# Kernel tuning notes

Hardware: AMD Instinct MI355X
Metric: run time of the kernel (lower is better)

## Reference

```python
import jax, jax.numpy as jnp
import numpy as np

B = 4096          # batch_size
D_EMB = 16        # per-side embedding dim (embed_to_from width = 2*D_EMB)
D_HIGH = 784      # flattened high-dim feature size
NSR = 5           # negative_sample_rate
A = 1.576943      # UMAP _a
B_PARAM = 0.8950608  # UMAP _b
REPULSION = 1.0
EPS = 1e-4
GLOBAL_LOSS = 0.5
TOTAL_STEPS = 1000
BATCH_COUNT = 500  # fixed step for deterministic alpha/beta
WARMUP = int(0.05 * TOTAL_STEPS)


def _safe_sqrt(sq):
    # sqrt with zero (not NaN) gradient at 0, matching zero-distance pairs
    safe = jnp.where(sq > 0, sq, 1.0)
    return jnp.where(sq > 0, jnp.sqrt(safe), 0.0)


def _pairwise_dist(x):
    # ||x_i - x_j|| via gram trick; avoids materializing [N,N,D]
    sq = jnp.sum(x * x, axis=1)                      # [N]
    gram = x @ x.T                                   # [N,N]
    d2 = sq[:, None] + sq[None, :] - 2.0 * gram
    return _safe_sqrt(jnp.maximum(d2, 0.0))


def _umap_ce_loss(embed_to_from, perm):
    e_to, e_from = jnp.split(embed_to_from, 2, axis=1)   # [B, D_EMB] each
    neg_to = jnp.repeat(e_to, NSR, axis=0)               # [B*NSR, D_EMB]
    repeat_neg = jnp.repeat(e_from, NSR, axis=0)
    neg_from = repeat_neg[perm]                          # shuffled negatives
    d_pos = _safe_sqrt(jnp.sum((e_to - e_from) ** 2, axis=1))
    d_neg = _safe_sqrt(jnp.sum((neg_to - neg_from) ** 2, axis=1))
    dist = jnp.concatenate([d_pos, d_neg], axis=0)       # [B*(1+NSR)]
    p_dist = 1.0 / (1.0 + A * dist ** (2.0 * B_PARAM))
    p_graph = jnp.concatenate([jnp.ones(B, p_dist.dtype), jnp.zeros(B * NSR, p_dist.dtype)])
    attraction = -p_graph * jnp.log(jnp.clip(p_dist, EPS, 1.0))
    repellant = -(1.0 - p_graph) * jnp.log(jnp.clip(1.0 - p_dist, EPS, 1.0)) * REPULSION
    return jnp.mean(attraction + repellant)


def _global_feature_loss(embed_to_from, to_x):
    e_to = embed_to_from[:, :D_EMB]
    to_x = to_x.reshape(to_x.shape[0], -1)
    high_dis = _pairwise_dist(to_x)     # [N,N]
    low_dis = _pairwise_dist(e_to)      # [N,N]
    # row-wise pearson correlation between high_dis and low_dis
    h = high_dis - jnp.mean(high_dis, axis=1, keepdims=True)
    l = low_dis - jnp.mean(low_dis, axis=1, keepdims=True)
    num = jnp.sum(h * l, axis=1)
    den = jnp.sqrt(jnp.sum(h * h, axis=1)) * jnp.sqrt(jnp.sum(l * l, axis=1))
    corr = jnp.mean(num / den)
    return -corr


def _alpha_beta():
    if BATCH_COUNT >= WARMUP:
        if BATCH_COUNT <= 0.9 * TOTAL_STEPS:
            beta = max(0.0, GLOBAL_LOSS * (1 - BATCH_COUNT / (TOTAL_STEPS - WARMUP * 4)) ** 2)
        else:
            beta = 0.0
        alpha = max(0.0, 1 - beta)
    else:
        alpha = 0.0
        beta = GLOBAL_LOSS
    return alpha, beta


def setup_inputs() -> dict:
    key = jax.random.key(0)
    k1, k2, k3 = jax.random.split(key, 3)
    embed_to_from = jax.random.normal(k1, (B, 2 * D_EMB), dtype=jnp.float32)
    placeholder = jax.random.normal(k2, (B, D_HIGH), dtype=jnp.float32)
    perm = jax.random.permutation(k3, B * NSR).astype(jnp.int32)
    return {"embed_to_from": embed_to_from, "placeholder": placeholder, "perm": perm}


def reference(embed_to_from, placeholder, perm):
    loss = _umap_ce_loss(embed_to_from, perm)
    loss_g = _global_feature_loss(embed_to_from, placeholder)
    alpha, beta = _alpha_beta()
    return alpha * loss + beta * loss_g
```

## Files before the change

### kernel.cpp

```cpp
#include <hip/hip_runtime.h>
#include <hip/hip_bf16.h>
#include <math.h>

#define NB    4096
#define DH    784
#define KX    800
#define NSR   5
#define NNEG  (NB*NSR)
#define NTOT  (NB + NNEG)

#define A_CONST 1.576943f
#define PEXP    1.7901216f
#define EPS_C   1.0e-4f
#define ALPHA_C 0.9296875f
#define BETA_C  0.0703125f

#define NSLOT 64
#define SLAB  (NB * NSLOT)
#define NBLK  528
#define BUFE  4096

typedef __hip_bfloat16 bf16;
typedef short bf16x8 __attribute__((ext_vector_type(8)));
typedef float f32x4  __attribute__((ext_vector_type(4)));

#define WS_XBF    0
#define WS_EBF    6553600
#define WS_SQX    6815744
#define WS_SQE    6832128
#define WS_STATSP 6848512
#define WS_UPART  12091392
#define WS_CPART  12091776

__device__ __forceinline__ void gl2lds16(const bf16* g, bf16* l) {
    __builtin_amdgcn_global_load_lds(
        (const __attribute__((address_space(1))) unsigned int*)g,
        (__attribute__((address_space(3))) unsigned int*)l,
        16, 0, 0);
}

__global__ void prep_fused(const float* __restrict__ X, const float* __restrict__ emb,
                           const int* __restrict__ perm, bf16* __restrict__ Xbf,
                           float* __restrict__ sqx, bf16* __restrict__ Ebf,
                           float* __restrict__ sqe, float* __restrict__ upart) {
    if (blockIdx.x < 1024) {
        const int wave = threadIdx.x >> 6, lane = threadIdx.x & 63;
        const int row = blockIdx.x * 4 + wave;
        const float4* xr = (const float4*)(X + (size_t)row * DH);
        bf16* xb = Xbf + (size_t)row * KX;
        float s = 0.f;
        #pragma unroll
        for (int it = 0; it < 4; ++it) {
            const int idx = lane + it * 64;
            if (idx < 196) {
                float4 v = xr[idx];
                s += v.x * v.x + v.y * v.y + v.z * v.z + v.w * v.w;
                union { bf16 h[4]; ushort4 u; } cv;
                cv.h[0] = __float2bfloat16(v.x);
                cv.h[1] = __float2bfloat16(v.y);
                cv.h[2] = __float2bfloat16(v.z);
                cv.h[3] = __float2bfloat16(v.w);
                *(ushort4*)(xb + idx * 4) = cv.u;
            }
        }
        if (lane < 16) xb[DH + lane] = __float2bfloat16(0.f);
        #pragma unroll
        for (int off = 32; off; off >>= 1) s += __shfl_down(s, off, 64);
        if (lane == 0) sqx[row] = s;
        return;
    }
    const int ub = blockIdx.x - 1024;
    const int t = ub * 256 + threadIdx.x;
    float val = 0.f;
    if (t < NB) {
        const float4* av = (const float4*)(emb + (size_t)t * 32);
        float4 t0 = av[0], t1 = av[1], t2 = av[2], t3 = av[3];
        float4 f0 = av[4], f1 = av[5], f2 = av[6], f3 = av[7];
        bf16* eb = Ebf + (size_t)t * 32;
        union { bf16 h[4]; ushort4 u; } cv;
        #define ST4(dst, q) cv.h[0]=__float2bfloat16(q.x); cv.h[1]=__float2bfloat16(q.y); \
                            cv.h[2]=__float2bfloat16(q.z); cv.h[3]=__float2bfloat16(q.w); \
                            *(ushort4*)(dst) = cv.u;
        ST4(eb,      t0) ST4(eb + 4,  t1) ST4(eb + 8,  t2) ST4(eb + 12, t3)
        #undef ST4
        ushort4 z = {0, 0, 0, 0};
        *(ushort4*)(eb + 16) = z; *(ushort4*)(eb + 20) = z;
        *(ushort4*)(eb + 24) = z; *(ushort4*)(eb + 28) = z;
        sqe[t] = t0.x*t0.x + t0.y*t0.y + t0.z*t0.z + t0.w*t0.w
               + t1.x*t1.x + t1.y*t1.y + t1.z*t1.z + t1.w*t1.w
               + t2.x*t2.x + t2.y*t2.y + t2.z*t2.z + t2.w*t2.w
               + t3.x*t3.x + t3.y*t3.y + t3.z*t3.z + t3.w*t3.w;
        float d2 = 0.f;
        #define D2(a, b) { float4 df = {a.x-b.x, a.y-b.y, a.z-b.z, a.w-b.w}; \
                           d2 += df.x*df.x + df.y*df.y + df.z*df.z + df.w*df.w; }
        D2(t0, f0) D2(t1, f1) D2(t2, f2) D2(t3, f3)
        #undef D2
        float d = sqrtf(d2);
        float p = 1.f / (1.f + A_CONST * powf(d, PEXP));
        val = -logf(fminf(fmaxf(p, EPS_C), 1.f));
    } else if (t < NTOT) {
        const int k = t - NB;
        const int ti = k / 5;
        const int fi = perm[k] / 5;
        const float4* at = (const float4*)(emb + (size_t)ti * 32);
        const float4* bt = (const float4*)(emb + (size_t)fi * 32 + 16);
        float d2 = 0.f;
        #pragma unroll
        for (int q = 0; q < 4; ++q) {
            float4 a = at[q], b = bt[q];
            float4 df = {a.x-b.x, a.y-b.y, a.z-b.z, a.w-b.w};
            d2 += df.x*df.x + df.y*df.y + df.z*df.z + df.w*df.w;
        }
        float d = sqrtf(d2);
        float p = 1.f / (1.f + A_CONST * powf(d, PEXP));
        val = -logf(fminf(fmaxf(1.f - p, EPS_C), 1.f));
    }
    #pragma unroll
    for (int off = 32; off; off >>= 1) val += __shfl_down(val, off, 64);
    __shared__ float ps[4];
    if ((threadIdx.x & 63) == 0) ps[threadIdx.x >> 6] = val;
    __syncthreads();
    if (threadIdx.x == 0) upart[ub] = ps[0] + ps[1] + ps[2] + ps[3];
}

__global__ __launch_bounds__(256, 3) void gram_kernel(
    const bf16* __restrict__ Xbf, const bf16* __restrict__ Ebf,
    const float* __restrict__ sqx, const float* __restrict__ sqe,
    float* __restrict__ statsp) {
    __shared__ bf16 As[2 * BUFE];
    __shared__ bf16 Bs[2 * BUFE];
    __shared__ float sqxs[256];
    __shared__ float sqes[256];

    int n = (blockIdx.x & 7) * 66 + (blockIdx.x >> 3);
    int bi = 0;
    while (n >= 32 - bi) { n -= 32 - bi; ++bi; }
    const int bj = bi + n;
    const int i0 = bi * 128, j0 = bj * 128;

    const int tid  = threadIdx.x;
    const int wave = tid >> 6;
    const int lane = tid & 63;
    const int wy = wave >> 1, wx = wave & 1;
    const int quad = lane >> 4, l15 = lane & 15;

    f32x4 acc[4][4];
    #pragma unroll
    for (int a = 0; a < 4; ++a)
        #pragma unroll
        for (int b = 0; b < 4; ++b)
            acc[a][b] = (f32x4){0.f, 0.f, 0.f, 0.f};

    const int c0  = wave * 2;
    const int rA  = lane >> 2;
    const int gseg = ((lane & 3) ^ ((lane >> 3) & 3)) * 8;

    const bf16* gA0 = Xbf + (size_t)(i0 + c0 * 16 + rA) * KX + gseg;
    const bf16* gA1 = Xbf + (size_t)(i0 + c0 * 16 + 16 + rA) * KX + gseg;
    const bf16* gB0 = Xbf + (size_t)(j0 + c0 * 16 + rA) * KX + gseg;
    const bf16* gB1 = Xbf + (size_t)(j0 + c0 * 16 + 16 + rA) * KX + gseg;

    gl2lds16(gA0, As + c0 * 512);
    gl2lds16(gA1, As + c0 * 512 + 512);
    gl2lds16(gB0, Bs + c0 * 512);
    gl2lds16(gB1, Bs + c0 * 512 + 512);
    gA0 += 32; gA1 += 32; gB0 += 32; gB1 += 32;

    if (tid < 128) {
        sqxs[tid] = sqx[i0 + tid]; sqxs[128 + tid] = sqx[j0 + tid];
        sqes[tid] = sqe[i0 + tid]; sqes[128 + tid] = sqe[j0 + tid];
    }

    const int posq = (quad ^ ((l15 >> 1) & 3)) * 8;

    for (int it = 0; it < 25; ++it) {
        __syncthreads();
        const int cur = (it & 1) * BUFE;
        const int nxt = ((it + 1) & 1) * BUFE;
        if (it < 24) {
            gl2lds16(gA0, As + nxt + c0 * 512);
            gl2lds16(gA1, As + nxt + c0 * 512 + 512);
            gl2lds16(gB0, Bs + nxt + c0 * 512);
            gl2lds16(gB1, Bs + nxt + c0 * 512 + 512);
            gA0 += 32; gA1 += 32; gB0 += 32; gB1 += 32;
        } else {
            gl2lds16(Ebf + (size_t)(i0 + c0 * 16 + rA) * 32 + gseg,      As + nxt + c0 * 512);
            gl2lds16(Ebf + (size_t)(i0 + c0 * 16 + 16 + rA) * 32 + gseg, As + nxt + c0 * 512 + 512);
            gl2lds16(Ebf + (size_t)(j0 + c0 * 16 + rA) * 32 + gseg,      Bs + nxt + c0 * 512);
            gl2lds16(Ebf + (size_t)(j0 + c0 * 16 + 16 + rA) * 32 + gseg, Bs + nxt + c0 * 512 + 512);
        }
        bf16x8 af[4], bfr[4];
        #pragma unroll
        for (int mi = 0; mi < 4; ++mi)
            af[mi] = *(const bf16x8*)&As[cur + (wy * 64 + mi * 16 + l15) * 32 + posq];
        #pragma unroll
        for (int ni = 0; ni < 4; ++ni)
            bfr[ni] = *(const bf16x8*)&Bs[cur + (wx * 64 + ni * 16 + l15) * 32 + posq];
        #pragma unroll
        for (int mi = 0; mi < 4; ++mi)
            #pragma unroll
            for (int ni = 0; ni < 4; ++ni)
                acc[mi][ni] = __builtin_amdgcn_mfma_f32_16x16x32_bf16(
                    af[mi], bfr[ni], acc[mi][ni], 0, 0, 0);
    }
    __syncthreads();

    const int slot_r = bj * 2 + wx;
    const int slot_c = bi * 2 + wy;
    bf16x8 bfrE[4];
    #pragma unroll
    for (int ni = 0; ni < 4; ++ni)
        bfrE[ni] = *(const bf16x8*)&Bs[BUFE + (wx * 64 + ni * 16 + l15) * 32 + posq];
    float cH[4] = {0,0,0,0}, cH2[4] = {0,0,0,0}, cL[4] = {0,0,0,0},
          cL2[4] = {0,0,0,0}, cHL[4] = {0,0,0,0};
    #pragma unroll
    for (int mi = 0; mi < 4; ++mi) {
        bf16x8 afE = *(const bf16x8*)&As[BUFE + (wy * 64 + mi * 16 + l15) * 32 + posq];
        f32x4 aE[4];
        #pragma unroll
        for (int ni = 0; ni < 4; ++ni) {
            f32x4 z = (f32x4){0.f, 0.f, 0.f, 0.f};
            aE[ni] = __builtin_amdgcn_mfma_f32_16x16x32_bf16(afE, bfrE[ni], z, 0, 0, 0);
        }
        const int ilocb = wy * 64 + mi * 16 + quad * 4;
        float sH[4] = {0,0,0,0}, sH2[4] = {0,0,0,0}, sL[4] = {0,0,0,0},
              sL2[4] = {0,0,0,0}, sHL[4] = {0,0,0,0};
        #pragma unroll
        for (int ni = 0; ni < 4; ++ni) {
            const int jloc = wx * 64 + ni * 16 + l15;
            const int j = j0 + jloc;
            const float sqxj = sqxs[128 + jloc];
            const float sqej = sqes[128 + jloc];
            #pragma unroll
            for (int r = 0; r < 4; ++r) {
                const int iloc = ilocb + r;
                const int i = i0 + iloc;
                float H, L;
                if (i == j) { H = 0.f; L = 0.f; }
                else {
                    float d2  = sqxs[iloc] + sqxj - 2.0f * acc[mi][ni][r];
                    H = sqrtf(fmaxf(d2, 0.f));
                    float d2e = sqes[iloc] + sqej - 2.0f * aE[ni][r];
                    L = sqrtf(fmaxf(d2e, 0.f));
                }
                sH[r] += H; sH2[r] += H * H; sL[r] += L; sL2[r] += L * L; sHL[r] += H * L;
                cH[ni] += H; cH2[ni] += H * H; cL[ni] += L; cL2[ni] += L * L; cHL[ni] += H * L;
            }
        }
        #pragma unroll
        for (int r = 0; r < 4; ++r) {
            float v0 = sH[r], v1 = sH2[r], v2 = sL[r], v3 = sL2[r], v4 = sHL[r];
            #pragma unroll
            for (int off = 1; off < 16; off <<= 1) {
                v0 += __shfl_xor(v0, off, 64);
                v1 += __shfl_xor(v1, off, 64);
                v2 += __shfl_xor(v2, off, 64);
                v3 += __shfl_xor(v3, off, 64);
                v4 += __shfl_xor(v4, off, 64);
            }
            if (l15 == 0) {
                const int i = i0 + ilocb + r;
                float* base = statsp + (size_t)slot_r * NB + i;
                base[0 * SLAB] = v0;
                base[1 * SLAB] = v1;
                base[2 * SLAB] = v2;
                base[3 * SLAB] = v3;
                base[4 * SLAB] = v4;
            }
        }
    }
    if (bi != bj) {
        #pragma unroll
        for (int ni = 0; ni < 4; ++ni) {
            float v0 = cH[ni], v1 = cH2[ni], v2 = cL[ni], v3 = cL2[ni], v4 = cHL[ni];
            #pragma unroll
            for (int off = 16; off < 64; off <<= 1) {
                v0 += __shfl_xor(v0, off, 64);
                v1 += __shfl_xor(v1, off, 64);
                v2 += __shfl_xor(v2, off, 64);
                v3 += __shfl_xor(v3, off, 64);
                v4 += __shfl_xor(v4, off, 64);
            }
            if (quad == 0) {
                const int j = j0 + wx * 64 + ni * 16 + l15;
                float* base = statsp + (size_t)slot_c * NB + j;
                base[0 * SLAB] = v0;
                base[1 * SLAB] = v1;
                base[2 * SLAB] = v2;
                base[3 * SLAB] = v3;
                base[4 * SLAB] = v4;
            }
        }
    }
}

__global__ void finish1_kernel(const float* __restrict__ statsp, float* __restrict__ cpart) {
    __shared__ float ps2[4][64][5];
    const int t = threadIdx.x;
    const int rloc = t & 63;
    const int sg = t >> 6;
    const int r = blockIdx.x * 64 + rloc;
    float sh = 0.f, sh2 = 0.f, sl = 0.f, sl2 = 0.f, shl = 0.f;
    for (int s = sg * 16; s < sg * 16 + 16; ++s) {
        const float* base = statsp + (size_t)s * NB + r;
        sh  += base[0 * SLAB];
        sh2 += base[1 * SLAB];
        sl  += base[2 * SLAB];
        sl2 += base[3 * SLAB];
        shl += base[4 * SLAB];
    }
    ps2[sg][rloc][0] = sh; ps2[sg][rloc][1] = sh2; ps2[sg][rloc][2] = sl;
    ps2[sg][rloc][3] = sl2; ps2[sg][rloc][4] = shl;
    __syncthreads();
    if (t < 64) {
        float a = 0.f, b = 0.f, c = 0.f, d = 0.f, e = 0.f;
        #pragma unroll
        for (int g = 0; g < 4; ++g) {
            a += ps2[g][t][0]; b += ps2[g][t][1]; c += ps2[g][t][2];
            d += ps2[g][t][3]; e += ps2[g][t][4];
        }
        const float invN = 1.0f / (float)NB;
        float num = e - a * c * invN;
        float vh  = fmaxf(b - a * a * invN, 0.f);
        float vl  = fmaxf(d - c * c * invN, 0.f);
        float local = num / (sqrtf(vh) * sqrtf(vl));
        #pragma unroll
        for (int off = 32; off; off >>= 1) local += __shfl_down(local, off, 64);
        if (t == 0) cpart[blockIdx.x] = local;
    }
}

__global__ void final_kernel(const float* __restrict__ cpart, const float* __restrict__ upart,
                             float* __restrict__ out) {
    const int t = threadIdx.x;
    float c = (t < 64) ? cpart[t] : 0.f;
    float u = (t < 96) ? upart[t] : 0.f;
    #pragma unroll
    for (int off = 32; off; off >>= 1) {
        c += __shfl_down(c, off, 64);
        u += __shfl_down(u, off, 64);
    }
    __shared__ float pc[2], pu[2];
    if ((t & 63) == 0) { pc[t >> 6] = c; pu[t >> 6] = u; }
    __syncthreads();
    if (t == 0) {
        float corr = (pc[0] + pc[1]) / (float)NB;
        float loss_g = -corr;
        float loss_u = (pu[0] + pu[1]) / (float)NTOT;
        out[0] = ALPHA_C * loss_u + BETA_C * loss_g;
    }
}

extern "C" void kernel_launch(void* const* d_in, const int* in_sizes, int n_in,
                              void* d_out, int out_size, void* d_ws, size_t ws_size,
                              hipStream_t stream) {
    const float* emb  = (const float*)d_in[0];
    const float* ph   = (const float*)d_in[1];
    const int*   perm = (const int*)d_in[2];
    float* out = (float*)d_out;

    char* ws = (char*)d_ws;
    bf16*  Xbf    = (bf16*) (ws + WS_XBF);
    bf16*  Ebf    = (bf16*) (ws + WS_EBF);
    float* sqx    = (float*)(ws + WS_SQX);
    float* sqe    = (float*)(ws + WS_SQE);
    float* statsp = (float*)(ws + WS_STATSP);
    float* upart  = (float*)(ws + WS_UPART);
    float* cpart  = (float*)(ws + WS_CPART);

    prep_fused<<<1120, 256, 0, stream>>>(ph, emb, perm, Xbf, sqx, Ebf, sqe, upart);
    gram_kernel<<<NBLK, 256, 0, stream>>>(Xbf, Ebf, sqx, sqe, statsp);
    finish1_kernel<<<64, 256, 0, stream>>>(statsp, cpart);
    final_kernel<<<1, 128, 0, stream>>>(cpart, upart, out);
}
```

Baseline: 123.2 us.

## Double K-tile to 64 in gram kernel, stagger K start, fuse final reduction

The gram kernel now loads 64-wide K slices per stage instead of 32, with a wider XOR swizzle. This halves the number of barrier-separated iterations and issues two MFMAs per fragment pair. The embedding tile is folded into the tail slice, and each block starts its K sweep at a different offset to spread memory traffic. The separate final reduction kernel is removed in favour of a last-block-done atomic counter in finish1, saving one launch. The cost is doubled LDS per block and launch bounds lowered from 3 to 2 blocks per CU, so occupancy drops.

```diff
diff --git a/kernel.cpp b/kernel.cpp
--- a/kernel.cpp
+++ b/kernel.cpp
@@ -18,7 +18,7 @@
 #define NSLOT 64
 #define SLAB  (NB * NSLOT)
 #define NBLK  528
-#define BUFE  4096
+#define BUFE  8192
 
 typedef __hip_bfloat16 bf16;
 typedef short bf16x8 __attribute__((ext_vector_type(8)));
@@ -31,6 +31,7 @@
 #define WS_STATSP 6848512
 #define WS_UPART  12091392
 #define WS_CPART  12091776
+#define WS_CNT    12092032
 
 __device__ __forceinline__ void gl2lds16(const bf16* g, bf16* l) {
     __builtin_amdgcn_global_load_lds(
@@ -42,7 +43,9 @@
 __global__ void prep_fused(const float* __restrict__ X, const float* __restrict__ emb,
                            const int* __restrict__ perm, bf16* __restrict__ Xbf,
                            float* __restrict__ sqx, bf16* __restrict__ Ebf,
-                           float* __restrict__ sqe, float* __restrict__ upart) {
+                           float* __restrict__ sqe, float* __restrict__ upart,
+                           unsigned* __restrict__ cnt) {
+    if (blockIdx.x == 0 && threadIdx.x == 0) *cnt = 0u;
     if (blockIdx.x < 1024) {
         const int wave = threadIdx.x >> 6, lane = threadIdx.x & 63;
         const int row = blockIdx.x * 4 + wave;
@@ -123,7 +126,7 @@
     if (threadIdx.x == 0) upart[ub] = ps[0] + ps[1] + ps[2] + ps[3];
 }
 
-__global__ __launch_bounds__(256, 3) void gram_kernel(
+__global__ __launch_bounds__(256, 2) void gram_kernel(
     const bf16* __restrict__ Xbf, const bf16* __restrict__ Ebf,
     const float* __restrict__ sqx, const float* __restrict__ sqe,
     float* __restrict__ statsp) {
@@ -137,6 +140,7 @@
     while (n >= 32 - bi) { n -= 32 - bi; ++bi; }
     const int bj = bi + n;
     const int i0 = bi * 128, j0 = bj * 128;
+    const int off = (bi * 5 + bj) % 12;
 
     const int tid  = threadIdx.x;
     const int wave = tid >> 6;
@@ -151,51 +155,89 @@
         for (int b = 0; b < 4; ++b)
             acc[a][b] = (f32x4){0.f, 0.f, 0.f, 0.f};
 
-    const int c0  = wave * 2;
-    const int rA  = lane >> 2;
-    const int gseg = ((lane & 3) ^ ((lane >> 3) & 3)) * 8;
-
-    const bf16* gA0 = Xbf + (size_t)(i0 + c0 * 16 + rA) * KX + gseg;
-    const bf16* gA1 = Xbf + (size_t)(i0 + c0 * 16 + 16 + rA) * KX + gseg;
-    const bf16* gB0 = Xbf + (size_t)(j0 + c0 * 16 + rA) * KX + gseg;
-    const bf16* gB1 = Xbf + (size_t)(j0 + c0 * 16 + 16 + rA) * KX + gseg;
-
-    gl2lds16(gA0, As + c0 * 512);
-    gl2lds16(gA1, As + c0 * 512 + 512);
-    gl2lds16(gB0, Bs + c0 * 512);
-    gl2lds16(gB1, Bs + c0 * 512 + 512);
-    gA0 += 32; gA1 += 32; gB0 += 32; gB1 += 32;
+    const int g0   = wave * 4;
+    const int lrow = lane >> 3;
+    const int sl   = (lane & 7) ^ (lrow & 7);
+
+    const bf16* pA[4]; const bf16* pB[4]; const bf16* tA[4]; const bf16* tB[4];
+    #pragma unroll
+    for (int g = 0; g < 4; ++g) {
+        const int rA = i0 + (g0 + g) * 8 + lrow;
+        const int rB = j0 + (g0 + g) * 8 + lrow;
+        pA[g] = Xbf + (size_t)rA * KX + sl * 8;
+        pB[g] = Xbf + (size_t)rB * KX + sl * 8;
+        tA[g] = (sl < 4) ? Xbf + (size_t)rA * KX + 768 + sl * 8
+                         : Ebf + (size_t)rA * 32 + (sl - 4) * 8;
+        tB[g] = (sl < 4) ? Xbf + (size_t)rB * KX + 768 + sl * 8
+                         : Ebf + (size_t)rB * 32 + (sl - 4) * 8;
+    }
+
+    #pragma unroll
+    for (int g = 0; g < 4; ++g) {
+        gl2lds16(pA[g] + off * 64, As + (g0 + g) * 512);
+        gl2lds16(pB[g] + off * 64, Bs + (g0 + g) * 512);
+    }
 
     if (tid < 128) {
         sqxs[tid] = sqx[i0 + tid]; sqxs[128 + tid] = sqx[j0 + tid];
         sqes[tid] = sqe[i0 + tid]; sqes[128 + tid] = sqe[j0 + tid];
     }
 
-    const int posq = (quad ^ ((l15 >> 1) & 3)) * 8;
-
-    for (int it = 0; it < 25; ++it) {
+    const int l7   = l15 & 7;
+    const int pos0 = (quad ^ l7) * 8;
+    const int pos1 = ((4 + quad) ^ l7) * 8;
+
+    for (int t = 0; t < 12; ++t) {
         __syncthreads();
-        const int cur = (it & 1) * BUFE;
-        const int nxt = ((it + 1) & 1) * BUFE;
-        if (it < 24) {
-            gl2lds16(gA0, As + nxt + c0 * 512);
-            gl2lds16(gA1, As + nxt + c0 * 512 + 512);
-            gl2lds16(gB0, Bs + nxt + c0 * 512);
-            gl2lds16(gB1, Bs + nxt + c0 * 512 + 512);
-            gA0 += 32; gA1 += 32; gB0 += 32; gB1 += 32;
+        const int cur = (t & 1) * BUFE;
+        const int nb  = ((t + 1) & 1) * BUFE;
+        if (t < 11) {
+            const int s = (t + 1 + off) % 12;
+            #pragma unroll
+            for (int g = 0; g < 4; ++g) {
+                gl2lds16(pA[g] + s * 64, As + nb + (g0 + g) * 512);
+                gl2lds16(pB[g] + s * 64, Bs + nb + (g0 + g) * 512);
+            }
         } else {
-            gl2lds16(Ebf + (size_t)(i0 + c0 * 16 + rA) * 32 + gseg,      As + nxt + c0 * 512);
-            gl2lds16(Ebf + (size_t)(i0 + c0 * 16 + 16 + rA) * 32 + gseg, As + nxt + c0 * 512 + 512);
-            gl2lds16(Ebf + (size_t)(j0 + c0 * 16 + rA) * 32 + gseg,      Bs + nxt + c0 * 512);
-            gl2lds16(Ebf + (size_t)(j0 + c0 * 16 + 16 + rA) * 32 + gseg, Bs + nxt + c0 * 512 + 512);
-        }
+            #pragma unroll
+            for (int g = 0; g < 4; ++g) {
+                gl2lds16(tA[g], As + nb + (g0 + g) * 512);
+                gl2lds16(tB[g], Bs + nb + (g0 + g) * 512);
+            }
+        }
+        bf16x8 af0[4], af1[4], bf0[4], bf1[4];
+        #pragma unroll
+        for (int mi = 0; mi < 4; ++mi) {
+            const int r = (wy * 64 + mi * 16 + l15) * 64;
+            af0[mi] = *(const bf16x8*)&As[cur + r + pos0];
+            af1[mi] = *(const bf16x8*)&As[cur + r + pos1];
+        }
+        #pragma unroll
+        for (int ni = 0; ni < 4; ++ni) {
+            const int r = (wx * 64 + ni * 16 + l15) * 64;
+            bf0[ni] = *(const bf16x8*)&Bs[cur + r + pos0];
+            bf1[ni] = *(const bf16x8*)&Bs[cur + r + pos1];
+        }
+        #pragma unroll
+        for (int mi = 0; mi < 4; ++mi)
+            #pragma unroll
+            for (int ni = 0; ni < 4; ++ni) {
+                acc[mi][ni] = __builtin_amdgcn_mfma_f32_16x16x32_bf16(
+                    af0[mi], bf0[ni], acc[mi][ni], 0, 0, 0);
+                acc[mi][ni] = __builtin_amdgcn_mfma_f32_16x16x32_bf16(
+                    af1[mi], bf1[ni], acc[mi][ni], 0, 0, 0);
+            }
+    }
+    __syncthreads();
+
+    {
         bf16x8 af[4], bfr[4];
         #pragma unroll
         for (int mi = 0; mi < 4; ++mi)
-            af[mi] = *(const bf16x8*)&As[cur + (wy * 64 + mi * 16 + l15) * 32 + posq];
+            af[mi] = *(const bf16x8*)&As[(wy * 64 + mi * 16 + l15) * 64 + pos0];
         #pragma unroll
         for (int ni = 0; ni < 4; ++ni)
-            bfr[ni] = *(const bf16x8*)&Bs[cur + (wx * 64 + ni * 16 + l15) * 32 + posq];
+            bfr[ni] = *(const bf16x8*)&Bs[(wx * 64 + ni * 16 + l15) * 64 + pos0];
         #pragma unroll
         for (int mi = 0; mi < 4; ++mi)
             #pragma unroll
@@ -203,19 +245,18 @@
                 acc[mi][ni] = __builtin_amdgcn_mfma_f32_16x16x32_bf16(
                     af[mi], bfr[ni], acc[mi][ni], 0, 0, 0);
     }
-    __syncthreads();
 
     const int slot_r = bj * 2 + wx;
     const int slot_c = bi * 2 + wy;
     bf16x8 bfrE[4];
     #pragma unroll
     for (int ni = 0; ni < 4; ++ni)
-        bfrE[ni] = *(const bf16x8*)&Bs[BUFE + (wx * 64 + ni * 16 + l15) * 32 + posq];
+        bfrE[ni] = *(const bf16x8*)&Bs[(wx * 64 + ni * 16 + l15) * 64 + pos1];
     float cH[4] = {0,0,0,0}, cH2[4] = {0,0,0,0}, cL[4] = {0,0,0,0},
           cL2[4] = {0,0,0,0}, cHL[4] = {0,0,0,0};
     #pragma unroll
     for (int mi = 0; mi < 4; ++mi) {
-        bf16x8 afE = *(const bf16x8*)&As[BUFE + (wy * 64 + mi * 16 + l15) * 32 + posq];
+        bf16x8 afE = *(const bf16x8*)&As[(wy * 64 + mi * 16 + l15) * 64 + pos1];
         f32x4 aE[4];
         #pragma unroll
         for (int ni = 0; ni < 4; ++ni) {
@@ -251,12 +292,12 @@
         for (int r = 0; r < 4; ++r) {
             float v0 = sH[r], v1 = sH2[r], v2 = sL[r], v3 = sL2[r], v4 = sHL[r];
             #pragma unroll
-            for (int off = 1; off < 16; off <<= 1) {
-                v0 += __shfl_xor(v0, off, 64);
-                v1 += __shfl_xor(v1, off, 64);
-                v2 += __shfl_xor(v2, off, 64);
-                v3 += __shfl_xor(v3, off, 64);
-                v4 += __shfl_xor(v4, off, 64);
+            for (int off2 = 1; off2 < 16; off2 <<= 1) {
+                v0 += __shfl_xor(v0, off2, 64);
+                v1 += __shfl_xor(v1, off2, 64);
+                v2 += __shfl_xor(v2, off2, 64);
+                v3 += __shfl_xor(v3, off2, 64);
+                v4 += __shfl_xor(v4, off2, 64);
             }
             if (l15 == 0) {
                 const int i = i0 + ilocb + r;
@@ -274,12 +315,12 @@
         for (int ni = 0; ni < 4; ++ni) {
             float v0 = cH[ni], v1 = cH2[ni], v2 = cL[ni], v3 = cL2[ni], v4 = cHL[ni];
             #pragma unroll
-            for (int off = 16; off < 64; off <<= 1) {
-                v0 += __shfl_xor(v0, off, 64);
-                v1 += __shfl_xor(v1, off, 64);
-                v2 += __shfl_xor(v2, off, 64);
-                v3 += __shfl_xor(v3, off, 64);
-                v4 += __shfl_xor(v4, off, 64);
+            for (int off2 = 16; off2 < 64; off2 <<= 1) {
+                v0 += __shfl_xor(v0, off2, 64);
+                v1 += __shfl_xor(v1, off2, 64);
+                v2 += __shfl_xor(v2, off2, 64);
+                v3 += __shfl_xor(v3, off2, 64);
+                v4 += __shfl_xor(v4, off2, 64);
             }
             if (quad == 0) {
                 const int j = j0 + wx * 64 + ni * 16 + l15;
@@ -294,7 +335,9 @@
     }
 }
 
-__global__ void finish1_kernel(const float* __restrict__ statsp, float* __restrict__ cpart) {
+__global__ void finish1_kernel(const float* __restrict__ statsp, const float* __restrict__ upart,
+                               float* __restrict__ cpart, unsigned* __restrict__ cnt,
+                               float* __restrict__ out) {
     __shared__ float ps2[4][64][5];
     const int t = threadIdx.x;
     const int rloc = t & 63;
@@ -328,26 +371,24 @@
         for (int off = 32; off; off >>= 1) local += __shfl_down(local, off, 64);
         if (t == 0) cpart[blockIdx.x] = local;
     }
-}
-
-__global__ void final_kernel(const float* __restrict__ cpart, const float* __restrict__ upart,
-                             float* __restrict__ out) {
-    const int t = threadIdx.x;
-    float c = (t < 64) ? cpart[t] : 0.f;
-    float u = (t < 96) ? upart[t] : 0.f;
-    #pragma unroll
-    for (int off = 32; off; off >>= 1) {
-        c += __shfl_down(c, off, 64);
-        u += __shfl_down(u, off, 64);
-    }
-    __shared__ float pc[2], pu[2];
-    if ((t & 63) == 0) { pc[t >> 6] = c; pu[t >> 6] = u; }
+    __shared__ int lastFlag;
+    if (t == 0) {
+        __threadfence();
+        unsigned prev = atomicAdd(cnt, 1u);
+        lastFlag = (prev == 63u);
+    }
     __syncthreads();
-    if (t == 0) {
-        float corr = (pc[0] + pc[1]) / (float)NB;
-        float loss_g = -corr;
-        float loss_u = (pu[0] + pu[1]) / (float)NTOT;
-        out[0] = ALPHA_C * loss_u + BETA_C * loss_g;
+    if (lastFlag) {
+        __threadfence();
+        float v = 0.f;
+        if (t < 64) v += cpart[t] * (-BETA_C / (float)NB);
+        if (t < 96) v += upart[t] * (ALPHA_C / (float)NTOT);
+        #pragma unroll
+        for (int off = 32; off; off >>= 1) v += __shfl_down(v, off, 64);
+        __shared__ float fin[4];
+        if ((t & 63) == 0) fin[t >> 6] = v;
+        __syncthreads();
+        if (t == 0) out[0] = fin[0] + fin[1] + fin[2] + fin[3];
     }
 }
 
@@ -367,9 +408,9 @@
     float* statsp = (float*)(ws + WS_STATSP);
     float* upart  = (float*)(ws + WS_UPART);
     float* cpart  = (float*)(ws + WS_CPART);
-
-    prep_fused<<<1120, 256, 0, stream>>>(ph, emb, perm, Xbf, sqx, Ebf, sqe, upart);
+    unsigned* cnt = (unsigned*)(ws + WS_CNT);
+
+    prep_fused<<<1120, 256, 0, stream>>>(ph, emb, perm, Xbf, sqx, Ebf, sqe, upart, cnt);
     gram_kernel<<<NBLK, 256, 0, stream>>>(Xbf, Ebf, sqx, sqe, statsp);
-    finish1_kernel<<<64, 256, 0, stream>>>(statsp, cpart);
-    final_kernel<<<1, 128, 0, stream>>>(cpart, upart, out);
+    finish1_kernel<<<64, 256, 0, stream>>>(statsp, upart, cpart, cnt, out);
 }
```

Result: slower. 134.6 us (+9.2%).
